# Kernel optimization log

Hardware: AMD Instinct MI355X
Metric: run time of the kernel (lower is better)

The kernel has to match this reference:

```python
import jax, jax.numpy as jnp
import numpy as np

BN_EPS = 1e-5


def setup_inputs() -> dict:
    key = jax.random.key(0)
    ks = jax.random.split(key, 8)
    N, H, OUT = 32 * 1024, 512, 32
    return {
        "x": jax.random.normal(ks[0], (N, 2), dtype=jnp.float32),
        "batch_size": 32,
        "Wq": jax.random.normal(ks[1], (2, H), dtype=jnp.float32) / np.sqrt(2.0),
        "Wk": jax.random.normal(ks[2], (2, H), dtype=jnp.float32) / np.sqrt(2.0),
        "Wv": jax.random.normal(ks[3], (2, H), dtype=jnp.float32) / np.sqrt(2.0),
        "bn_gamma": jnp.ones((H,), jnp.float32),
        "bn_beta": jnp.zeros((H,), jnp.float32),
        "bn_mean": jnp.zeros((H,), jnp.float32),
        "bn_var": jnp.ones((H,), jnp.float32),
        "prelu_a": jnp.full((1,), 0.25, jnp.float32),
        "W_out": jax.random.normal(ks[4], (H, OUT), dtype=jnp.float32) / np.sqrt(H),
        "b_out": jnp.zeros((OUT,), jnp.float32),
    }


def reference(x, batch_size, Wq, Wk, Wv, bn_gamma, bn_beta, bn_mean, bn_var,
              prelu_a, W_out, b_out):
    H = Wq.shape[1]
    # project tokens [N,2] -> [B,S,H]
    q = (x @ Wq).reshape(batch_size, -1, H)
    k = (x @ Wk).reshape(batch_size, -1, H)
    v = (x @ Wv).reshape(batch_size, -1, H)
    scale = 1.0 / jnp.sqrt(jnp.asarray(H, x.dtype))
    attn = jax.nn.softmax(jnp.einsum("bqh,bkh->bqk", q, k) * scale, axis=-1)
    out = jnp.einsum("bqk,bkh->bqh", attn, v).reshape(-1, H)  # [N,H]
    # BatchNorm1d (eval mode) + PReLU + Linear (dropout = identity in eval)
    out = (out - bn_mean) * (bn_gamma / jnp.sqrt(bn_var + BN_EPS)) + bn_beta
    out = jnp.where(out >= 0, out, prelu_a[0] * out)
    return out @ W_out + b_out
```

## Files before the change

kernel.cpp:

```cpp
#include <hip/hip_runtime.h>
#include <math.h>


#define H_DIM   512
#define OUT_DIM 32
#define S_LEN   1024
#define THREADS 256
#define NW 4

#define WS_WOUT 0
#define WS_ABC  32768
#define WS_M    40960

#if __has_builtin(__builtin_amdgcn_exp2f)
#define EXP2(x) __builtin_amdgcn_exp2f(x)
#else
#define EXP2(x) exp2f(x)
#endif

typedef __attribute__((ext_vector_type(8))) short bf16x8;
typedef __attribute__((ext_vector_type(4))) float f32x4;

__device__ __forceinline__ unsigned int rne_bf16(float f) {
    unsigned int u = __float_as_uint(f);
    return (u + 0x7fffu + ((u >> 16) & 1u)) >> 16;
}
__device__ __forceinline__ unsigned int pack2bf16(float lo, float hi) {
    return rne_bf16(lo) | (rne_bf16(hi) << 16);
}

union frag_cast { unsigned int u[4]; int4 i4; bf16x8 v; };

__global__ __launch_bounds__(256)
void setup_kernel(const float* __restrict__ Wq, const float* __restrict__ Wk,
                  const float* __restrict__ Wv,
                  const float* __restrict__ gam, const float* __restrict__ bet,
                  const float* __restrict__ mean, const float* __restrict__ var,
                  const float* __restrict__ Wout,
                  unsigned char* __restrict__ ws)
{
    const int t = threadIdx.x;
    if (blockIdx.x < 16) {
        unsigned int* dst = (unsigned int*)(ws + WS_WOUT);
        #pragma unroll
        for (int k = 0; k < 2; ++k) {
            int pi = blockIdx.x * 512 + k * 256 + t;
            int d  = pi * 2;
            int fid = d >> 9;
            int l   = (d >> 3) & 63;
            int j   = d & 7;
            int nt  = fid >> 4;
            int s   = fid & 15;
            int h   = s * 32 + (l >> 4) * 8 + j;
            int o   = nt * 16 + (l & 15);
            float f0 = Wout[h * 32 + o];
            float f1 = Wout[(h + 1) * 32 + o];
            dst[pi] = pack2bf16(f0, f1);
        }
    } else {
        float4* abc = (float4*)(ws + WS_ABC);
        #pragma unroll
        for (int k = 0; k < 2; ++k) {
            int h = t + k * 256;
            float g = gam[h] * rsqrtf(var[h] + 1e-5f);
            abc[h] = make_float4(Wv[h] * g, Wv[H_DIM + h] * g,
                                 bet[h] - mean[h] * g, 0.f);
        }
        if (t < 64) {
            float m00 = 0.f, m01 = 0.f, m10 = 0.f, m11 = 0.f;
            #pragma unroll
            for (int k = 0; k < 8; ++k) {
                int h = t + k * 64;
                float a0 = Wq[h], a1 = Wq[H_DIM + h];
                float b0 = Wk[h], b1 = Wk[H_DIM + h];
                m00 = fmaf(a0, b0, m00); m01 = fmaf(a0, b1, m01);
                m10 = fmaf(a1, b0, m10); m11 = fmaf(a1, b1, m11);
            }
            #pragma unroll
            for (int off = 32; off >= 1; off >>= 1) {
                m00 += __shfl_xor(m00, off); m01 += __shfl_xor(m01, off);
                m10 += __shfl_xor(m10, off); m11 += __shfl_xor(m11, off);
            }
            if (t == 0) {
                const float scale = 0.044194173824159216f;
                float* m = (float*)(ws + WS_M);
                m[0] = m00 * scale; m[1] = m01 * scale;
                m[2] = m10 * scale; m[3] = m11 * scale;
            }
        }
    }
}

__global__ __launch_bounds__(THREADS)
void fused_attn_kernel(const float* __restrict__ x,
                       const float* __restrict__ prelu_a,
                       const float* __restrict__ bout,
                       const unsigned char* __restrict__ ws,
                       float* __restrict__ out)
{
    __shared__ float4 abcs[H_DIM];
    __shared__ float redl[NW][64], redw0[NW][64], redw1[NW][64];

    const int t    = threadIdx.x;
    const int lane = t & 63;
    const int q    = __builtin_amdgcn_readfirstlane(t >> 6);
    const int b    = blockIdx.x >> 4;
    const int tile = blockIdx.x & 15;
    const float L2E = 1.4426950408889634f;

    const float4* abcg = (const float4*)(ws + WS_ABC);
    abcs[t]       = abcg[t];
    abcs[t + 256] = abcg[t + 256];

    const float* mp = (const float*)(ws + WS_M);
    const float m00 = mp[0], m01 = mp[1], m10 = mp[2], m11 = mp[3];

    const float2 xt = ((const float2*)x)[b * S_LEN + tile * 64 + lane];
    const float u0L = fmaf(xt.x, m00, xt.y * m10) * L2E;
    const float u1L = fmaf(xt.x, m01, xt.y * m11) * L2E;

    float l = 0.f, w0 = 0.f, w1 = 0.f;
    const float4* kg = ((const float4*)x) + (size_t)b * (S_LEN / 2) + q * 128;
    #pragma unroll 8
    for (int i = 0; i < 128; ++i) {
        float4 k2 = kg[i];
        float e0 = EXP2(fmaf(u0L, k2.x, u1L * k2.y));
        float e1 = EXP2(fmaf(u0L, k2.z, u1L * k2.w));
        l += e0 + e1;
        w0 = fmaf(e0, k2.x, fmaf(e1, k2.z, w0));
        w1 = fmaf(e0, k2.y, fmaf(e1, k2.w, w1));
    }
    redl[q][lane] = l; redw0[q][lane] = w0; redw1[q][lane] = w1;
    __syncthreads();
    l  = redl[0][lane]  + redl[1][lane]  + redl[2][lane]  + redl[3][lane];
    w0 = redw0[0][lane] + redw0[1][lane] + redw0[2][lane] + redw0[3][lane];
    w1 = redw1[0][lane] + redw1[1][lane] + redw1[2][lane] + redw1[3][lane];
    const float inv = 1.0f / l;
    w0 *= inv; w1 *= inv;

    const int src = q * 16 + (lane & 15);
    const float w0t = __shfl(w0, src);
    const float w1t = __shfl(w1, src);

    const float ap = prelu_a[0];
    const int quad = lane >> 4;
    f32x4 acc0 = {0.f, 0.f, 0.f, 0.f};
    f32x4 acc1 = {0.f, 0.f, 0.f, 0.f};
    const int4* bsrc = (const int4*)(ws + WS_WOUT);

    #pragma unroll 4
    for (int s = 0; s < 16; ++s) {
        frag_cast bf0, bf1;
        bf0.i4 = bsrc[s * 64 + lane];
        bf1.i4 = bsrc[(16 + s) * 64 + lane];
        const int hbase = s * 32 + quad * 8;
        frag_cast af;
        #pragma unroll
        for (int jj = 0; jj < 4; ++jj) {
            float4 c0 = abcs[hbase + jj * 2];
            float4 c1 = abcs[hbase + jj * 2 + 1];
            float z0 = fmaf(w0t, c0.x, fmaf(w1t, c0.y, c0.z));
            float z1 = fmaf(w0t, c1.x, fmaf(w1t, c1.y, c1.z));
            float p0 = fmaxf(z0, 0.f) + ap * fminf(z0, 0.f);
            float p1 = fmaxf(z1, 0.f) + ap * fminf(z1, 0.f);
            af.u[jj] = pack2bf16(p0, p1);
        }
        acc0 = __builtin_amdgcn_mfma_f32_16x16x32_bf16(af.v, bf0.v, acc0, 0, 0, 0);
        acc1 = __builtin_amdgcn_mfma_f32_16x16x32_bf16(af.v, bf1.v, acc1, 0, 0, 0);
    }

    const size_t base = (size_t)(b * S_LEN + tile * 64) * OUT_DIM;
    const int o0 = lane & 15;
    const float bo0 = bout[o0], bo1 = bout[16 + o0];
    #pragma unroll
    for (int r = 0; r < 4; ++r) {
        const int tt = q * 16 + quad * 4 + r;
        out[base + tt * 32 + o0]      = acc0[r] + bo0;
        out[base + tt * 32 + 16 + o0] = acc1[r] + bo1;
    }
}

extern "C" void kernel_launch(void* const* d_in, const int* in_sizes, int n_in,
                              void* d_out, int out_size, void* d_ws, size_t ws_size,
                              hipStream_t stream) {
    const float* x    = (const float*)d_in[0];
    const float* Wq   = (const float*)d_in[2];
    const float* Wk   = (const float*)d_in[3];
    const float* Wv   = (const float*)d_in[4];
    const float* gam  = (const float*)d_in[5];
    const float* bet  = (const float*)d_in[6];
    const float* mean = (const float*)d_in[7];
    const float* var  = (const float*)d_in[8];
    const float* pa   = (const float*)d_in[9];
    const float* Wout = (const float*)d_in[10];
    const float* bo   = (const float*)d_in[11];
    float* out = (float*)d_out;
    unsigned char* ws = (unsigned char*)d_ws;

    hipLaunchKernelGGL(setup_kernel, dim3(17), dim3(256), 0, stream,
                       Wq, Wk, Wv, gam, bet, mean, var, Wout, ws);

    const int N = in_sizes[0] / 2;
    const int blocks = N / 64;
    hipLaunchKernelGGL(fused_attn_kernel, dim3(blocks), dim3(THREADS), 0, stream,
                       x, pa, bo, ws, out);
}
```

Measured before the change: 94.71 us.

## Halve tokens per block, split key range and hidden dim across waves

```diff
diff --git a/kernel.cpp b/kernel.cpp
--- a/kernel.cpp
+++ b/kernel.cpp
@@ -5,6 +5,7 @@
 #define H_DIM   512
 #define OUT_DIM 32
 #define S_LEN   1024
+#define TOK     32
 #define THREADS 256
 #define NW 4
 
@@ -99,30 +100,38 @@
                        float* __restrict__ out)
 {
     __shared__ float4 abcs[H_DIM];
-    __shared__ float redl[NW][64], redw0[NW][64], redw1[NW][64];
+    __shared__ float redl[NW][32], redw0[NW][32], redw1[NW][32];
+    __shared__ float yout[TOK][33];
 
     const int t    = threadIdx.x;
     const int lane = t & 63;
     const int q    = __builtin_amdgcn_readfirstlane(t >> 6);
-    const int b    = blockIdx.x >> 4;
-    const int tile = blockIdx.x & 15;
+    const int b    = blockIdx.x >> 5;
+    const int tile = blockIdx.x & 31;
     const float L2E = 1.4426950408889634f;
 
     const float4* abcg = (const float4*)(ws + WS_ABC);
     abcs[t]       = abcg[t];
     abcs[t + 256] = abcg[t + 256];
+    {
+        float* yflat = &yout[0][0];
+        #pragma unroll
+        for (int i = t; i < TOK * 33; i += THREADS) yflat[i] = 0.f;
+    }
 
     const float* mp = (const float*)(ws + WS_M);
     const float m00 = mp[0], m01 = mp[1], m10 = mp[2], m11 = mp[3];
 
-    const float2 xt = ((const float2*)x)[b * S_LEN + tile * 64 + lane];
+    const int tok = lane & 31;
+    const float2 xt = ((const float2*)x)[b * S_LEN + tile * TOK + tok];
     const float u0L = fmaf(xt.x, m00, xt.y * m10) * L2E;
     const float u1L = fmaf(xt.x, m01, xt.y * m11) * L2E;
 
     float l = 0.f, w0 = 0.f, w1 = 0.f;
-    const float4* kg = ((const float4*)x) + (size_t)b * (S_LEN / 2) + q * 128;
+    const int slice = q * 2 + (lane >> 5);
+    const float4* kg = ((const float4*)x) + (size_t)b * (S_LEN / 2) + slice * 64;
     #pragma unroll 8
-    for (int i = 0; i < 128; ++i) {
+    for (int i = 0; i < 64; ++i) {
         float4 k2 = kg[i];
         float e0 = EXP2(fmaf(u0L, k2.x, u1L * k2.y));
         float e1 = EXP2(fmaf(u0L, k2.z, u1L * k2.w));
@@ -130,15 +139,23 @@
         w0 = fmaf(e0, k2.x, fmaf(e1, k2.z, w0));
         w1 = fmaf(e0, k2.y, fmaf(e1, k2.w, w1));
     }
-    redl[q][lane] = l; redw0[q][lane] = w0; redw1[q][lane] = w1;
+    l  += __shfl_xor(l, 32);
+    w0 += __shfl_xor(w0, 32);
+    w1 += __shfl_xor(w1, 32);
+    if (lane < 32) { redl[q][lane] = l; redw0[q][lane] = w0; redw1[q][lane] = w1; }
     __syncthreads();
-    l  = redl[0][lane]  + redl[1][lane]  + redl[2][lane]  + redl[3][lane];
-    w0 = redw0[0][lane] + redw0[1][lane] + redw0[2][lane] + redw0[3][lane];
-    w1 = redw1[0][lane] + redw1[1][lane] + redw1[2][lane] + redw1[3][lane];
+    l = 0.f; w0 = 0.f; w1 = 0.f;
+    #pragma unroll
+    for (int w = 0; w < NW; ++w) {
+        l  += redl[w][tok];
+        w0 += redw0[w][tok];
+        w1 += redw1[w][tok];
+    }
     const float inv = 1.0f / l;
     w0 *= inv; w1 *= inv;
 
-    const int src = q * 16 + (lane & 15);
+    const int tt = q & 1, kh = q >> 1;
+    const int src = tt * 16 + (lane & 15);
     const float w0t = __shfl(w0, src);
     const float w1t = __shfl(w1, src);
 
@@ -149,7 +166,8 @@
     const int4* bsrc = (const int4*)(ws + WS_WOUT);
 
     #pragma unroll 4
-    for (int s = 0; s < 16; ++s) {
+    for (int si = 0; si < 8; ++si) {
+        const int s = kh * 8 + si;
         frag_cast bf0, bf1;
         bf0.i4 = bsrc[s * 64 + lane];
         bf1.i4 = bsrc[(16 + s) * 64 + lane];
@@ -169,14 +187,25 @@
         acc1 = __builtin_amdgcn_mfma_f32_16x16x32_bf16(af.v, bf1.v, acc1, 0, 0, 0);
     }
 
-    const size_t base = (size_t)(b * S_LEN + tile * 64) * OUT_DIM;
     const int o0 = lane & 15;
-    const float bo0 = bout[o0], bo1 = bout[16 + o0];
     #pragma unroll
     for (int r = 0; r < 4; ++r) {
-        const int tt = q * 16 + quad * 4 + r;
-        out[base + tt * 32 + o0]      = acc0[r] + bo0;
-        out[base + tt * 32 + 16 + o0] = acc1[r] + bo1;
+        const int tk = tt * 16 + quad * 4 + r;
+        atomicAdd(&yout[tk][o0],      acc0[r]);
+        atomicAdd(&yout[tk][16 + o0], acc1[r]);
+    }
+    __syncthreads();
+
+    {
+        const size_t base = (size_t)(b * S_LEN + tile * TOK) * OUT_DIM;
+        const int tk = t >> 3, oq = t & 7;
+        const float4 b4 = ((const float4*)bout)[oq];
+        float4 v;
+        v.x = yout[tk][oq * 4 + 0] + b4.x;
+        v.y = yout[tk][oq * 4 + 1] + b4.y;
+        v.z = yout[tk][oq * 4 + 2] + b4.z;
+        v.w = yout[tk][oq * 4 + 3] + b4.w;
+        *(float4*)(out + base + (size_t)t * 4) = v;
     }
 }
 
@@ -201,7 +230,7 @@
                        Wq, Wk, Wv, gam, bet, mean, var, Wout, ws);
 
     const int N = in_sizes[0] / 2;
-    const int blocks = N / 64;
+    const int blocks = N / TOK;
     hipLaunchKernelGGL(fused_attn_kernel, dim3(blocks), dim3(THREADS), 0, stream,
                        x, pa, bo, ws, out);
 }
```

Measured after the change: 103.2 us. 1.09x slower.

## Split key loop across lane groups within a wave and drop shared-memory reduction

Applied to the files above, without the earlier changes.

```diff
diff --git a/kernel.cpp b/kernel.cpp
--- a/kernel.cpp
+++ b/kernel.cpp
@@ -6,7 +6,6 @@
 #define OUT_DIM 32
 #define S_LEN   1024
 #define THREADS 256
-#define NW 4
 
 #define WS_WOUT 0
 #define WS_ABC  32768
@@ -98,9 +97,6 @@
                        const unsigned char* __restrict__ ws,
                        float* __restrict__ out)
 {
-    __shared__ float4 abcs[H_DIM];
-    __shared__ float redl[NW][64], redw0[NW][64], redw1[NW][64];
-
     const int t    = threadIdx.x;
     const int lane = t & 63;
     const int q    = __builtin_amdgcn_readfirstlane(t >> 6);
@@ -108,19 +104,18 @@
     const int tile = blockIdx.x & 15;
     const float L2E = 1.4426950408889634f;
 
-    const float4* abcg = (const float4*)(ws + WS_ABC);
-    abcs[t]       = abcg[t];
-    abcs[t + 256] = abcg[t + 256];
+    const int m   = lane & 15;
+    const int sub = lane >> 4;
 
     const float* mp = (const float*)(ws + WS_M);
     const float m00 = mp[0], m01 = mp[1], m10 = mp[2], m11 = mp[3];
 
-    const float2 xt = ((const float2*)x)[b * S_LEN + tile * 64 + lane];
+    const float2 xt = ((const float2*)x)[b * S_LEN + tile * 64 + q * 16 + m];
     const float u0L = fmaf(xt.x, m00, xt.y * m10) * L2E;
     const float u1L = fmaf(xt.x, m01, xt.y * m11) * L2E;
 
     float l = 0.f, w0 = 0.f, w1 = 0.f;
-    const float4* kg = ((const float4*)x) + (size_t)b * (S_LEN / 2) + q * 128;
+    const float4* kg = ((const float4*)x) + (size_t)b * (S_LEN / 2) + sub * 128;
     #pragma unroll 8
     for (int i = 0; i < 128; ++i) {
         float4 k2 = kg[i];
@@ -130,35 +125,29 @@
         w0 = fmaf(e0, k2.x, fmaf(e1, k2.z, w0));
         w1 = fmaf(e0, k2.y, fmaf(e1, k2.w, w1));
     }
-    redl[q][lane] = l; redw0[q][lane] = w0; redw1[q][lane] = w1;
-    __syncthreads();
-    l  = redl[0][lane]  + redl[1][lane]  + redl[2][lane]  + redl[3][lane];
-    w0 = redw0[0][lane] + redw0[1][lane] + redw0[2][lane] + redw0[3][lane];
-    w1 = redw1[0][lane] + redw1[1][lane] + redw1[2][lane] + redw1[3][lane];
+    l  += __shfl_xor(l, 16);  l  += __shfl_xor(l, 32);
+    w0 += __shfl_xor(w0, 16); w0 += __shfl_xor(w0, 32);
+    w1 += __shfl_xor(w1, 16); w1 += __shfl_xor(w1, 32);
     const float inv = 1.0f / l;
-    w0 *= inv; w1 *= inv;
-
-    const int src = q * 16 + (lane & 15);
-    const float w0t = __shfl(w0, src);
-    const float w1t = __shfl(w1, src);
+    const float w0t = w0 * inv, w1t = w1 * inv;
 
     const float ap = prelu_a[0];
-    const int quad = lane >> 4;
     f32x4 acc0 = {0.f, 0.f, 0.f, 0.f};
     f32x4 acc1 = {0.f, 0.f, 0.f, 0.f};
-    const int4* bsrc = (const int4*)(ws + WS_WOUT);
+    const int4*   bsrc = (const int4*)(ws + WS_WOUT);
+    const float4* abcg = (const float4*)(ws + WS_ABC);
 
     #pragma unroll 4
     for (int s = 0; s < 16; ++s) {
         frag_cast bf0, bf1;
         bf0.i4 = bsrc[s * 64 + lane];
         bf1.i4 = bsrc[(16 + s) * 64 + lane];
-        const int hbase = s * 32 + quad * 8;
+        const int hbase = s * 32 + sub * 8;
         frag_cast af;
         #pragma unroll
         for (int jj = 0; jj < 4; ++jj) {
-            float4 c0 = abcs[hbase + jj * 2];
-            float4 c1 = abcs[hbase + jj * 2 + 1];
+            float4 c0 = abcg[hbase + jj * 2];
+            float4 c1 = abcg[hbase + jj * 2 + 1];
             float z0 = fmaf(w0t, c0.x, fmaf(w1t, c0.y, c0.z));
             float z1 = fmaf(w0t, c1.x, fmaf(w1t, c1.y, c1.z));
             float p0 = fmaxf(z0, 0.f) + ap * fminf(z0, 0.f);
@@ -170,11 +159,11 @@
     }
 
     const size_t base = (size_t)(b * S_LEN + tile * 64) * OUT_DIM;
-    const int o0 = lane & 15;
+    const int o0 = m;
     const float bo0 = bout[o0], bo1 = bout[16 + o0];
     #pragma unroll
     for (int r = 0; r < 4; ++r) {
-        const int tt = q * 16 + quad * 4 + r;
+        const int tt = q * 16 + sub * 4 + r;
         out[base + tt * 32 + o0]      = acc0[r] + bo0;
         out[base + tt * 32 + 16 + o0] = acc1[r] + bo1;
     }
```

Measured after the change: 96.01 us. No clear change (+1.4%).
